# Optimization experiments

Hardware: AMD Instinct MI355X
Metric: run time of the kernel (lower is better)

## Reference

```python
import jax, jax.numpy as jnp
import numpy as np

B, T, D, H, HD = 128, 256, 512, 8, 64

def setup_inputs() -> dict:
    key = jax.random.key(0)
    ks = jax.random.split(key, 5)
    scale = 0.02
    return {
        "x": jax.random.normal(ks[0], (B, T, D), dtype=jnp.float32),
        "Wq": jax.random.normal(ks[1], (H, D, HD), dtype=jnp.float32) * scale,
        "Wk": jax.random.normal(ks[2], (H, D, HD), dtype=jnp.float32) * scale,
        "Wv": jax.random.normal(ks[3], (H, D, HD), dtype=jnp.float32) * scale,
        "Wo": jax.random.normal(ks[4], (D, D), dtype=jnp.float32) * scale,
        "bo": jnp.zeros((D,), dtype=jnp.float32),
    }

def reference(x, Wq, Wk, Wv, Wo, bo):
    # Per-head projections, batched over heads: [B,T,D] x [H,D,HD] -> [B,H,T,HD]
    q = jnp.einsum('btd,hdk->bhtk', x, Wq)
    k = jnp.einsum('btd,hdk->bhtk', x, Wk)
    v = jnp.einsum('btd,hdk->bhtk', x, Wv)
    # Scaled scores [B,H,T,T] with causal mask
    scores = jnp.einsum('bhtk,bhsk->bhts', q, k) * (HD ** -0.5)
    causal = jnp.tril(jnp.ones((T, T), dtype=bool))
    scores = jnp.where(causal, scores, jnp.finfo(scores.dtype).min)
    attn = jax.nn.softmax(scores, axis=-1)
    # Dropout is identity at inference.
    out = jnp.einsum('bhts,bhsk->bhtk', attn, v)
    # Concat heads: [B,T,H*HD] == [B,T,D]
    out = out.transpose(0, 2, 1, 3).reshape(B, T, D)
    # Output projection
    return out @ Wo + bo
```

## Files before the change

### kernel.cpp

```cpp
#include <hip/hip_runtime.h>
#include <hip/hip_bf16.h>

typedef __bf16 bf16x8 __attribute__((ext_vector_type(8)));
typedef __bf16 bf16x4 __attribute__((ext_vector_type(4)));
typedef float f32x4 __attribute__((ext_vector_type(4)));
typedef unsigned short u16x8 __attribute__((ext_vector_type(8)));


__device__ __forceinline__ unsigned short f2bf(float f) {
  unsigned u = __float_as_uint(f);
  u += 0x7fffu + ((u >> 16) & 1u);
  return (unsigned short)(u >> 16);
}

__device__ __forceinline__ bf16x4 cvt4(f32x4 v) {
  bf16x4 o;
  o[0] = (__bf16)v[0]; o[1] = (__bf16)v[1]; o[2] = (__bf16)v[2]; o[3] = (__bf16)v[3];
  return o;
}

__device__ __forceinline__ void async16(const void* g, void* l) {
  __builtin_amdgcn_global_load_lds(
      (const __attribute__((address_space(1))) void*)g,
      (__attribute__((address_space(3))) void*)l, 16, 0, 0);
}

__global__ __launch_bounds__(256) void k_convert_x(const float* __restrict__ in,
                                                   unsigned short* __restrict__ out) {
  int i = blockIdx.x * 256 + threadIdx.x;
  const float4* p = (const float4*)in + (size_t)i * 2;
  float4 a = p[0], b = p[1];
  u16x8 o;
  o[0] = f2bf(a.x); o[1] = f2bf(a.y); o[2] = f2bf(a.z); o[3] = f2bf(a.w);
  o[4] = f2bf(b.x); o[5] = f2bf(b.y); o[6] = f2bf(b.z); o[7] = f2bf(b.w);
  *((u16x8*)out + i) = o;
}

__global__ __launch_bounds__(256) void k_transpose_w3(const float* __restrict__ w0,
                                                      const float* __restrict__ w1,
                                                      const float* __restrict__ w2,
                                                      unsigned short* __restrict__ out) {
  __shared__ unsigned short tile[64][72];
  int z = blockIdx.z;
  int wsel = z >> 3, hsel = z & 7;
  const float* inb = (wsel == 0 ? w0 : (wsel == 1 ? w1 : w2)) + (size_t)hsel * 512 * 64;
  unsigned short* outb = out + (size_t)z * 512 * 64;
  int r0 = blockIdx.y * 64;
  int tid = threadIdx.x;
  int r = tid >> 2, cq = (tid & 3) * 16;
  const float* src = inb + (size_t)(r0 + r) * 64 + cq;
#pragma unroll
  for (int i = 0; i < 16; i += 4) {
    float4 v = *(const float4*)(src + i);
    tile[r][cq + i + 0] = f2bf(v.x);
    tile[r][cq + i + 1] = f2bf(v.y);
    tile[r][cq + i + 2] = f2bf(v.z);
    tile[r][cq + i + 3] = f2bf(v.w);
  }
  __syncthreads();
  int cr = tid >> 2, rq = (tid & 3) * 16;
  u16x8 o0, o1;
#pragma unroll
  for (int i = 0; i < 8; ++i) o0[i] = tile[rq + i][cr];
#pragma unroll
  for (int i = 0; i < 8; ++i) o1[i] = tile[rq + 8 + i][cr];
  unsigned short* dst = outb + (size_t)cr * 512 + r0 + rq;
  *(u16x8*)dst = o0;
  *(u16x8*)(dst + 8) = o1;
}

__global__ __launch_bounds__(256) void k_transpose_w(const float* __restrict__ in,
                                                     unsigned short* __restrict__ out,
                                                     int rows, int cols) {
  __shared__ unsigned short tile[64][72];
  int c0 = blockIdx.x * 64, r0 = blockIdx.y * 64;
  int tid = threadIdx.x;
  int r = tid >> 2, cq = (tid & 3) * 16;
  const float* src = in + (size_t)(r0 + r) * cols + c0 + cq;
#pragma unroll
  for (int i = 0; i < 16; i += 4) {
    float4 v = *(const float4*)(src + i);
    tile[r][cq + i + 0] = f2bf(v.x);
    tile[r][cq + i + 1] = f2bf(v.y);
    tile[r][cq + i + 2] = f2bf(v.z);
    tile[r][cq + i + 3] = f2bf(v.w);
  }
  __syncthreads();
  int cr = tid >> 2, rq = (tid & 3) * 16;
  u16x8 o0, o1;
#pragma unroll
  for (int i = 0; i < 8; ++i) o0[i] = tile[rq + i][cr];
#pragma unroll
  for (int i = 0; i < 8; ++i) o1[i] = tile[rq + 8 + i][cr];
  unsigned short* dst = out + (size_t)(c0 + cr) * rows + r0 + rq;
  *(u16x8*)dst = o0;
  *(u16x8*)(dst + 8) = o1;
}

template <int KIND>
__global__ __launch_bounds__(512, 1) void k_gemmP(
    const unsigned short* __restrict__ A,
    const unsigned short* __restrict__ Bmat,
    unsigned short* __restrict__ O0,
    unsigned short* __restrict__ O1,
    const float* __restrict__ bo,
    float* __restrict__ outf) {
  __shared__ unsigned short smem[65536];
  const int P = (KIND == 0) ? 64 : 32;
  int xcd = blockIdx.x & 7, g = blockIdx.x >> 3;
  int w = xcd * P + g;
  int mt, nt;
  if (KIND == 0) { mt = w >> 2; nt = w & 3; }
  else           { mt = w >> 1; nt = w & 1; }
  int m0 = mt * 256, n0 = nt * 256;
  int tid = threadIdx.x;
  int wid = tid >> 6, lane = tid & 63;
  int lr = lane & 15, lg = lane >> 4;
  int wm = wid >> 2, wn = wid & 3;

  int srow_off = wid * 16 + (lane >> 3);
  int schunk = (lane & 7) ^ (lane >> 3);
  auto stageA = [&](int kb, int buf, int half) {
#pragma unroll
    for (int j = 0; j < 2; ++j) {
      int row = half * 128 + srow_off + j * 8;
      async16(A + (size_t)(m0 + row) * 512 + kb * 64 + schunk * 8,
              smem + buf * 32768 + half * 8192 + (wid * 2 + j) * 512);
    }
  };
  auto stageB = [&](int kb, int buf, int half) {
#pragma unroll
    for (int j = 0; j < 2; ++j) {
      int row = half * 128 + srow_off + j * 8;
      async16(Bmat + (size_t)(n0 + row) * 512 + kb * 64 + schunk * 8,
              smem + buf * 32768 + 16384 + half * 8192 + (wid * 2 + j) * 512);
    }
  };
  auto lda = [&](int buf, int mi, int k32) -> bf16x8 {
    int row = mi * 32 + wm * 16 + lr;
    int ch = (k32 * 4 + lg) ^ (lr & 7);
    return *(const bf16x8*)&smem[buf * 32768 + row * 64 + ch * 8];
  };
  auto ldb = [&](int buf, int ni, int k32) -> bf16x8 {
    int row = ni * 64 + wn * 16 + lr;
    int ch = (k32 * 4 + lg) ^ (lr & 7);
    return *(const bf16x8*)&smem[buf * 32768 + 16384 + row * 64 + ch * 8];
  };

  f32x4 acc[8][4];
#pragma unroll
  for (int mi = 0; mi < 8; ++mi)
#pragma unroll
    for (int ni = 0; ni < 4; ++ni) acc[mi][ni] = (f32x4){0.f, 0.f, 0.f, 0.f};

#define MF(dst, afrag, bfrag)                                                        \
  if constexpr (KIND == 2)                                                           \
    dst = __builtin_amdgcn_mfma_f32_16x16x32_bf16(afrag, bfrag, dst, 0, 0, 0);       \
  else                                                                               \
    dst = __builtin_amdgcn_mfma_f32_16x16x32_bf16(bfrag, afrag, dst, 0, 0, 0);

  stageA(0, 0, 0); stageB(0, 0, 0); stageA(0, 0, 1); stageB(0, 0, 1);
  asm volatile("s_waitcnt vmcnt(4)" ::: "memory");
  __builtin_amdgcn_s_barrier();
  asm volatile("" ::: "memory");

  bf16x8 a03[4][2], a47[4][2], b01[2][2], b23[2][2];
#pragma unroll
  for (int t = 0; t < 8; ++t) {
    int buf = t & 1, nbuf = buf ^ 1;
    const bool st = (t < 7);
#pragma unroll
    for (int mi = 0; mi < 4; ++mi) { a03[mi][0] = lda(buf, mi, 0); a03[mi][1] = lda(buf, mi, 1); }
#pragma unroll
    for (int ni = 0; ni < 2; ++ni) { b01[ni][0] = ldb(buf, ni, 0); b01[ni][1] = ldb(buf, ni, 1); }
    if (st) stageA(t + 1, nbuf, 0);
    asm volatile("" ::: "memory");
    __builtin_amdgcn_s_setprio(1);
#pragma unroll
    for (int mi = 0; mi < 4; ++mi)
#pragma unroll
      for (int ni = 0; ni < 2; ++ni)
#pragma unroll
        for (int k = 0; k < 2; ++k) { MF(acc[mi][ni], a03[mi][k], b01[ni][k]); }
    __builtin_amdgcn_s_setprio(0);
    if (st) asm volatile("s_waitcnt vmcnt(4)" ::: "memory");
    else    asm volatile("s_waitcnt vmcnt(2)" ::: "memory");
    __builtin_amdgcn_s_barrier();
    asm volatile("" ::: "memory");
#pragma unroll
    for (int mi = 0; mi < 4; ++mi) { a47[mi][0] = lda(buf, mi + 4, 0); a47[mi][1] = lda(buf, mi + 4, 1); }
    if (st) stageB(t + 1, nbuf, 0);
    asm volatile("" ::: "memory");
    __builtin_amdgcn_s_setprio(1);
#pragma unroll
    for (int mi = 0; mi < 4; ++mi)
#pragma unroll
      for (int ni = 0; ni < 2; ++ni)
#pragma unroll
        for (int k = 0; k < 2; ++k) { MF(acc[mi + 4][ni], a47[mi][k], b01[ni][k]); }
    __builtin_amdgcn_s_setprio(0);
    if (st) asm volatile("s_waitcnt vmcnt(4)" ::: "memory");
    else    asm volatile("s_waitcnt vmcnt(0)" ::: "memory");
    __builtin_amdgcn_s_barrier();
    asm volatile("" ::: "memory");
#pragma unroll
    for (int ni = 0; ni < 2; ++ni) { b23[ni][0] = ldb(buf, ni + 2, 0); b23[ni][1] = ldb(buf, ni + 2, 1); }
    if (st) stageA(t + 1, nbuf, 1);
    asm volatile("" ::: "memory");
    __builtin_amdgcn_s_setprio(1);
#pragma unroll
    for (int mi = 0; mi < 4; ++mi)
#pragma unroll
      for (int ni = 0; ni < 2; ++ni)
#pragma unroll
        for (int k = 0; k < 2; ++k) { MF(acc[mi + 4][ni + 2], a47[mi][k], b23[ni][k]); }
    __builtin_amdgcn_s_setprio(0);
    __builtin_amdgcn_s_barrier();
    asm volatile("" ::: "memory");
    if (st) stageB(t + 1, nbuf, 1);
    asm volatile("" ::: "memory");
    __builtin_amdgcn_s_setprio(1);
#pragma unroll
    for (int mi = 0; mi < 4; ++mi)
#pragma unroll
      for (int ni = 0; ni < 2; ++ni)
#pragma unroll
        for (int k = 0; k < 2; ++k) { MF(acc[mi][ni + 2], a03[mi][k], b23[ni][k]); }
    __builtin_amdgcn_s_setprio(0);
    if (st) asm volatile("s_waitcnt vmcnt(4)" ::: "memory");
    __builtin_amdgcn_s_barrier();
    asm volatile("" ::: "memory");
  }
#undef MF

  if constexpr (KIND == 0) {
    int z = n0 >> 9;
    int hbase = (n0 & 511) >> 6;
    int hd0 = wn * 16 + lg * 4;
#pragma unroll
    for (int ni = 0; ni < 4; ++ni) {
      unsigned short* outp = (z ? O1 : O0) + (size_t)(mt * 8 + hbase + ni) * 16384;
#pragma unroll
      for (int mi = 0; mi < 8; ++mi) {
        int tq = mi * 32 + wm * 16 + lr;
        *(bf16x4*)&outp[(size_t)tq * 64 + hd0] = cvt4(acc[mi][ni]);
      }
    }
  } else if constexpr (KIND == 1) {
#pragma unroll
    for (int ni = 0; ni < 4; ++ni) {
      int nb = n0 + ni * 64 + wn * 16 + lg * 4;
      float4 b4 = *(const float4*)&bo[nb];
#pragma unroll
      for (int mi = 0; mi < 8; ++mi) {
        int mg = m0 + mi * 32 + wm * 16 + lr;
        float4 o;
        o.x = acc[mi][ni][0] + b4.x; o.y = acc[mi][ni][1] + b4.y;
        o.z = acc[mi][ni][2] + b4.z; o.w = acc[mi][ni][3] + b4.w;
        *(float4*)&outf[(size_t)mg * 512 + nb] = o;
      }
    }
  } else {
    int hbase = n0 >> 6;
    int hd = wn * 16 + lr;
#pragma unroll
    for (int ni = 0; ni < 4; ++ni) {
      unsigned short* outp = O0 + (size_t)(mt * 8 + hbase + ni) * 16384;
#pragma unroll
      for (int mi = 0; mi < 8; ++mi) {
        int tq = mi * 32 + wm * 16 + lg * 4;
        *(bf16x4*)&outp[(size_t)hd * 256 + tq] = cvt4(acc[mi][ni]);
      }
    }
  }
}

__global__ __launch_bounds__(512, 4) void k_attn2(
    const unsigned short* __restrict__ Qb,
    const unsigned short* __restrict__ Kb,
    const unsigned short* __restrict__ Vtb,
    unsigned short* __restrict__ Ob) {
  __shared__ unsigned short Ks[16384];
  __shared__ unsigned short Vs[16384];
  __shared__ unsigned short Ps[8][16][36];
  int bh = blockIdx.x;
  int tid = threadIdx.x, wid = tid >> 6, lane = tid & 63, lr = lane & 15, lg = lane >> 4;
  int bb = bh >> 3, h = bh & 7;
  const unsigned short* Kg = Kb + (size_t)bh * 16384;
  const unsigned short* Vg = Vtb + (size_t)bh * 16384;
#pragma unroll
  for (int c = 0; c < 4; ++c) {
    int d = (wid * 4 + c) * 64 + lane;
    int kr = d >> 3, kc = (d & 7) ^ (kr & 7);
    async16(Kg + (size_t)kr * 64 + kc * 8, Ks + (wid * 4 + c) * 512);
    int vr = d >> 5, vc = (d & 31) ^ ((vr & 7) << 2);
    async16(Vg + (size_t)vr * 256 + vc * 8, Vs + (wid * 4 + c) * 512);
  }
  __syncthreads();

#pragma unroll
  for (int cc = 0; cc < 2; ++cc) {
    int ci = cc ? (15 - wid) : wid;
    int t0 = ci * 16, trow = t0 + lr;
    int ntV = ci + 1;
    int ntE = (ntV + 1) & ~1;
    int nk32 = ntE >> 1;
    const unsigned short* qsrc = Qb + (size_t)bh * 16384 + (size_t)(t0 + lr) * 64 + lg * 8;
    bf16x8 bq0 = *(const bf16x8*)qsrc;
    bf16x8 bq1 = *(const bf16x8*)(qsrc + 32);
    f32x4 acc[16];
#pragma unroll
    for (int nt = 0; nt < 16; ++nt)
      if (nt < ntE) acc[nt] = (f32x4){0.f, 0.f, 0.f, 0.f};
#pragma unroll
    for (int nt = 0; nt < 16; ++nt)
      if (nt < ntV) {
        int row = nt * 16 + lr;
        bf16x8 ak0 = *(const bf16x8*)&Ks[row * 64 + ((0 + lg) ^ (lr & 7)) * 8];
        acc[nt] = __builtin_amdgcn_mfma_f32_16x16x32_bf16(ak0, bq0, acc[nt], 0, 0, 0);
        bf16x8 ak1 = *(const bf16x8*)&Ks[row * 64 + ((4 + lg) ^ (lr & 7)) * 8];
        acc[nt] = __builtin_amdgcn_mfma_f32_16x16x32_bf16(ak1, bq1, acc[nt], 0, 0, 0);
      }
    float m = -3.0e38f;
#pragma unroll
    for (int nt = 0; nt < 16; ++nt)
      if (nt < ntE) {
#pragma unroll
        for (int r = 0; r < 4; ++r) {
          float v = acc[nt][r] * 0.125f;
          if (nt * 16 + lg * 4 + r > trow) v = -1.0e30f;
          acc[nt][r] = v;
          m = fmaxf(m, v);
        }
      }
    m = fmaxf(m, __shfl_xor(m, 16));
    m = fmaxf(m, __shfl_xor(m, 32));
    float s = 0.f;
    bf16x4 pk[16];
#pragma unroll
    for (int nt = 0; nt < 16; ++nt)
      if (nt < ntE) {
#pragma unroll
        for (int r = 0; r < 4; ++r) {
          float p = __expf(acc[nt][r] - m);
          s += p;
          pk[nt][r] = (__bf16)p;
        }
      }
    s += __shfl_xor(s, 16);
    s += __shfl_xor(s, 32);
    float inv = 1.0f / s;
    *(bf16x4*)&Ps[wid][lr][lg * 4] = pk[0];
    *(bf16x4*)&Ps[wid][lr][16 + lg * 4] = pk[1];
    f32x4 aco[4];
#pragma unroll
    for (int vt = 0; vt < 4; ++vt) aco[vt] = (f32x4){0.f, 0.f, 0.f, 0.f};
#pragma unroll
    for (int k32 = 0; k32 < 8; ++k32)
      if (k32 < nk32) {
        bf16x8 pb = *(const bf16x8*)&Ps[wid][lr][lg * 8];
        if (k32 + 1 < nk32) {
          *(bf16x4*)&Ps[wid][lr][lg * 4] = pk[2 * k32 + 2];
          *(bf16x4*)&Ps[wid][lr][16 + lg * 4] = pk[2 * k32 + 3];
        }
#pragma unroll
        for (int vt = 0; vt < 4; ++vt) {
          int row = vt * 16 + lr;
          bf16x8 av = *(const bf16x8*)&Vs[row * 256 + (((k32 * 4 + lg) ^ ((lr & 7) << 2)) * 8)];
          aco[vt] = __builtin_amdgcn_mfma_f32_16x16x32_bf16(av, pb, aco[vt], 0, 0, 0);
        }
      }
    unsigned short* obase = Ob + (size_t)(bb * 256 + trow) * 512 + h * 64 + lg * 4;
#pragma unroll
    for (int vt = 0; vt < 4; ++vt) {
      bf16x4 ov;
#pragma unroll
      for (int r = 0; r < 4; ++r) ov[r] = (__bf16)(aco[vt][r] * inv);
      *(bf16x4*)(obase + vt * 16) = ov;
    }
  }
}

extern "C" void kernel_launch(void* const* d_in, const int* in_sizes, int n_in,
                              void* d_out, int out_size, void* d_ws, size_t ws_size,
                              hipStream_t stream) {
  (void)in_sizes; (void)n_in; (void)out_size; (void)ws_size;
  const float* x = (const float*)d_in[0];
  const float* Wq = (const float*)d_in[1];
  const float* Wk = (const float*)d_in[2];
  const float* Wv = (const float*)d_in[3];
  const float* Wo = (const float*)d_in[4];
  const float* bo = (const float*)d_in[5];
  float* out = (float*)d_out;
  char* ws = (char*)d_ws;
  const size_t MB = 1024 * 1024;
  unsigned short* Qb = (unsigned short*)(ws);
  unsigned short* Kb = (unsigned short*)(ws + 32 * MB);
  unsigned short* Vtb = (unsigned short*)(ws + 64 * MB);
  unsigned short* xb = (unsigned short*)(ws + 96 * MB);
  unsigned short* Wqt = (unsigned short*)(ws + 128 * MB);
  unsigned short* Wkt = Wqt + 262144;
  unsigned short* Wvt = Wkt + 262144;
  unsigned short* Wot = Wvt + 262144;

  hipLaunchKernelGGL(k_convert_x, dim3(8192), dim3(256), 0, stream, x, xb);
  hipLaunchKernelGGL(k_transpose_w3, dim3(1, 8, 24), dim3(256), 0, stream, Wq, Wk, Wv, Wqt);
  hipLaunchKernelGGL(k_transpose_w, dim3(8, 8, 1), dim3(256), 0, stream, Wo, Wot, 512, 512);
  hipLaunchKernelGGL((k_gemmP<0>), dim3(512), dim3(512), 0, stream,
                     xb, Wqt, Qb, Kb, (const float*)nullptr, (float*)nullptr);
  hipLaunchKernelGGL((k_gemmP<2>), dim3(256), dim3(512), 0, stream,
                     xb, Wvt, Vtb, (unsigned short*)nullptr, (const float*)nullptr, (float*)nullptr);
  hipLaunchKernelGGL(k_attn2, dim3(1024), dim3(512), 0, stream, Qb, Kb, Vtb, xb);
  hipLaunchKernelGGL((k_gemmP<1>), dim3(256), dim3(512), 0, stream,
                     xb, Wot, (unsigned short*)nullptr, (unsigned short*)nullptr, bo, out);
}
```

Before: 168.3 us.

## Overlap V tile load with QK^T and fold softmax scale into Q projection

The Q projection output is pre-scaled by log2(e)/sqrt(HD), so the attention kernel can use exp2f with no per-element scale. The K and V async loads are split and waited on separately, letting the first chunk's QK^T and softmax run while V is still in flight. Q fragments for both chunks are loaded up front. The causal mask now applies only to the diagonal tile, the padded odd tile is skipped with zeroed P values, and the row sum uses four partial accumulators. The vmcnt counts are hand-tuned, so correctness depends on the exact order in which loads are issued.

```diff
diff --git a/kernel.cpp b/kernel.cpp
--- a/kernel.cpp
+++ b/kernel.cpp
@@ -235,6 +235,12 @@
 
   if constexpr (KIND == 0) {
     int z = n0 >> 9;
+    if (z == 0) {
+#pragma unroll
+      for (int mi = 0; mi < 8; ++mi)
+#pragma unroll
+        for (int ni = 0; ni < 4; ++ni) acc[mi][ni] *= 0.18033688011112042f;
+    }
     int hbase = (n0 & 511) >> 6;
     int hd0 = wn * 16 + lg * 4;
 #pragma unroll
@@ -293,63 +299,84 @@
     int d = (wid * 4 + c) * 64 + lane;
     int kr = d >> 3, kc = (d & 7) ^ (kr & 7);
     async16(Kg + (size_t)kr * 64 + kc * 8, Ks + (wid * 4 + c) * 512);
+  }
+  int ci0 = wid, ci1 = 15 - wid;
+  const unsigned short* q0 = Qb + (size_t)bh * 16384 + (size_t)(ci0 * 16 + lr) * 64 + lg * 8;
+  const unsigned short* q1 = Qb + (size_t)bh * 16384 + (size_t)(ci1 * 16 + lr) * 64 + lg * 8;
+  bf16x8 bq0a = *(const bf16x8*)q0;
+  bf16x8 bq0b = *(const bf16x8*)(q0 + 32);
+  bf16x8 bq1a = *(const bf16x8*)q1;
+  bf16x8 bq1b = *(const bf16x8*)(q1 + 32);
+#pragma unroll
+  for (int c = 0; c < 4; ++c) {
+    int d = (wid * 4 + c) * 64 + lane;
     int vr = d >> 5, vc = (d & 31) ^ ((vr & 7) << 2);
     async16(Vg + (size_t)vr * 256 + vc * 8, Vs + (wid * 4 + c) * 512);
   }
-  __syncthreads();
-
-#pragma unroll
-  for (int cc = 0; cc < 2; ++cc) {
-    int ci = cc ? (15 - wid) : wid;
+  asm volatile("s_waitcnt vmcnt(4)" ::: "memory");
+  __builtin_amdgcn_s_barrier();
+  asm volatile("" ::: "memory");
+
+  auto do_chunk = [&](int ci, bf16x8 bqa, bf16x8 bqb, bool waitV) {
     int t0 = ci * 16, trow = t0 + lr;
     int ntV = ci + 1;
     int ntE = (ntV + 1) & ~1;
     int nk32 = ntE >> 1;
-    const unsigned short* qsrc = Qb + (size_t)bh * 16384 + (size_t)(t0 + lr) * 64 + lg * 8;
-    bf16x8 bq0 = *(const bf16x8*)qsrc;
-    bf16x8 bq1 = *(const bf16x8*)(qsrc + 32);
     f32x4 acc[16];
-#pragma unroll
-    for (int nt = 0; nt < 16; ++nt)
-      if (nt < ntE) acc[nt] = (f32x4){0.f, 0.f, 0.f, 0.f};
 #pragma unroll
     for (int nt = 0; nt < 16; ++nt)
       if (nt < ntV) {
+        acc[nt] = (f32x4){0.f, 0.f, 0.f, 0.f};
         int row = nt * 16 + lr;
         bf16x8 ak0 = *(const bf16x8*)&Ks[row * 64 + ((0 + lg) ^ (lr & 7)) * 8];
-        acc[nt] = __builtin_amdgcn_mfma_f32_16x16x32_bf16(ak0, bq0, acc[nt], 0, 0, 0);
+        acc[nt] = __builtin_amdgcn_mfma_f32_16x16x32_bf16(ak0, bqa, acc[nt], 0, 0, 0);
         bf16x8 ak1 = *(const bf16x8*)&Ks[row * 64 + ((4 + lg) ^ (lr & 7)) * 8];
-        acc[nt] = __builtin_amdgcn_mfma_f32_16x16x32_bf16(ak1, bq1, acc[nt], 0, 0, 0);
+        acc[nt] = __builtin_amdgcn_mfma_f32_16x16x32_bf16(ak1, bqb, acc[nt], 0, 0, 0);
       }
     float m = -3.0e38f;
 #pragma unroll
     for (int nt = 0; nt < 16; ++nt)
-      if (nt < ntE) {
-#pragma unroll
-        for (int r = 0; r < 4; ++r) {
-          float v = acc[nt][r] * 0.125f;
-          if (nt * 16 + lg * 4 + r > trow) v = -1.0e30f;
-          acc[nt][r] = v;
-          m = fmaxf(m, v);
+      if (nt < ntV) {
+        if (nt == ci) {
+#pragma unroll
+          for (int r = 0; r < 4; ++r) {
+            float v = acc[nt][r];
+            if (lg * 4 + r > lr) v = -1.0e30f;
+            acc[nt][r] = v;
+            m = fmaxf(m, v);
+          }
+        } else {
+#pragma unroll
+          for (int r = 0; r < 4; ++r) m = fmaxf(m, acc[nt][r]);
         }
       }
     m = fmaxf(m, __shfl_xor(m, 16));
     m = fmaxf(m, __shfl_xor(m, 32));
-    float s = 0.f;
+    float s4[4] = {0.f, 0.f, 0.f, 0.f};
     bf16x4 pk[16];
 #pragma unroll
     for (int nt = 0; nt < 16; ++nt)
-      if (nt < ntE) {
+      if (nt < ntV) {
 #pragma unroll
         for (int r = 0; r < 4; ++r) {
-          float p = __expf(acc[nt][r] - m);
-          s += p;
+          float p = exp2f(acc[nt][r] - m);
+          s4[r] += p;
           pk[nt][r] = (__bf16)p;
         }
       }
+    if (ntV & 1) {
+      pk[ntV][0] = (__bf16)0.f; pk[ntV][1] = (__bf16)0.f;
+      pk[ntV][2] = (__bf16)0.f; pk[ntV][3] = (__bf16)0.f;
+    }
+    float s = (s4[0] + s4[1]) + (s4[2] + s4[3]);
     s += __shfl_xor(s, 16);
     s += __shfl_xor(s, 32);
     float inv = 1.0f / s;
+    if (waitV) {
+      asm volatile("s_waitcnt vmcnt(0)" ::: "memory");
+      __builtin_amdgcn_s_barrier();
+      asm volatile("" ::: "memory");
+    }
     *(bf16x4*)&Ps[wid][lr][lg * 4] = pk[0];
     *(bf16x4*)&Ps[wid][lr][16 + lg * 4] = pk[1];
     f32x4 aco[4];
@@ -378,7 +405,10 @@
       for (int r = 0; r < 4; ++r) ov[r] = (__bf16)(aco[vt][r] * inv);
       *(bf16x4*)(obase + vt * 16) = ov;
     }
-  }
+  };
+
+  do_chunk(ci0, bq0a, bq0b, true);
+  do_chunk(ci1, bq1a, bq1b, false);
 }
 
 extern "C" void kernel_launch(void* const* d_in, const int* in_sizes, int n_in,
```

Measured after the change: 169.3 us. About the same (+0.6%).
